# Kernel optimization log

Measured on AMD Instinct MI355X. Metric: run time of the kernel, lower is better.

Reference implementation:

```python
import jax, jax.numpy as jnp
import numpy as np

DIM = 1024
HEADS = 16
HEAD_DIM = DIM // HEADS
B, N = 2, 2048


def setup_inputs() -> dict:
    key = jax.random.key(0)
    ks = jax.random.split(key, 5)
    s = 1.0 / np.sqrt(DIM)
    return {
        "x": jax.random.normal(ks[0], (B, N, DIM), dtype=jnp.float32),
        "W_qkv": jax.random.uniform(ks[1], (DIM, 3 * DIM), jnp.float32, -s, s),
        "b_qkv": jax.random.uniform(ks[2], (3 * DIM,), jnp.float32, -s, s),
        "W_out": jax.random.uniform(ks[3], (DIM, DIM), jnp.float32, -s, s),
        "b_out": jax.random.uniform(ks[4], (DIM,), jnp.float32, -s, s),
    }


def reference(x, W_qkv, b_qkv, W_out, b_out):
    Bx, Nx, D = x.shape
    qkv = x @ W_qkv + b_qkv  # [B, N, 3D]
    qkv = qkv.reshape(Bx, Nx, 3, HEADS, HEAD_DIM)
    q, k, v = jnp.moveaxis(qkv, 2, 0)  # each [B, N, H, hd]
    q = jnp.swapaxes(q, 1, 2)  # [B, H, N, hd]
    k = jnp.swapaxes(k, 1, 2)
    v = jnp.swapaxes(v, 1, 2)
    scale = 1.0 / np.sqrt(HEAD_DIM)
    attn = jnp.einsum("bhqd,bhkd->bhqk", q, k) * scale  # [B, H, N, N]
    attn = jax.nn.softmax(attn, axis=-1)
    ctx = jnp.einsum("bhqk,bhkd->bhqd", attn, v)  # [B, H, N, hd]
    ctx = jnp.swapaxes(ctx, 1, 2).reshape(Bx, Nx, D)
    return ctx @ W_out + b_out
```

## Files before the change

### kernel.cpp

```cpp
#include <hip/hip_runtime.h>
#include <hip/hip_bf16.h>
#include <hip/hip_fp16.h>

#define DIMSZ 1024
#define HEADS 16
#define HD 64
#define BATCH 2
#define SEQ 2048
#define MROWS (BATCH*SEQ)

typedef _Float16 f16;
typedef _Float16 f16x8 __attribute__((ext_vector_type(8)));
typedef float f32x4 __attribute__((ext_vector_type(4)));

__device__ __forceinline__ void gload_lds16(const void* g, void* l) {
  __builtin_amdgcn_global_load_lds(
      (const __attribute__((address_space(1))) unsigned int*)g,
      (__attribute__((address_space(3))) unsigned int*)l, 16, 0, 0);
}

__global__ __launch_bounds__(256) void k_cvt_x(const float* __restrict__ in,
                                               f16* __restrict__ out) {
  int i = blockIdx.x * 256 + threadIdx.x;
  float4 v = ((const float4*)in)[i];
  union { f16 h[4]; uint2 u; } p;
  p.h[0] = (f16)v.x; p.h[1] = (f16)v.y; p.h[2] = (f16)v.z; p.h[3] = (f16)v.w;
  ((uint2*)out)[i] = p.u;
}

__global__ __launch_bounds__(256) void k_tcvt(const float* __restrict__ in,
                                              f16* __restrict__ out,
                                              int R, int C) {
  __shared__ f16 t[64][66];
  int c0 = blockIdx.x * 64, r0 = blockIdx.y * 64;
  int tid = threadIdx.x;
  int cc = tid & 63;
  #pragma unroll
  for (int p = 0; p < 16; p++) {
    int r = p * 4 + (tid >> 6);
    t[r][cc] = (f16)in[(size_t)(r0 + r) * C + c0 + cc];
  }
  __syncthreads();
  int rr = tid & 63;
  #pragma unroll
  for (int p = 0; p < 16; p++) {
    int c = p * 4 + (tid >> 6);
    out[(size_t)(c0 + c) * R + r0 + rr] = t[rr][c];
  }
}

#define GEMM_CORE(Aptr, Bptr)                                                  \
  __shared__ __align__(16) f16 As[128 * 64];                                   \
  __shared__ __align__(16) f16 Bs[128 * 64];                                   \
  const int K = 1024;                                                          \
  int tid = threadIdx.x, l = tid & 63, w = tid >> 6;                           \
  int bm = blockIdx.y, bn = blockIdx.x;                                        \
  int wr = (w >> 1) * 64, wc = (w & 1) * 64;                                   \
  const f16* Ag = (Aptr) + (size_t)bm * 128 * K;                               \
  const f16* Bg = (Bptr) + (size_t)bn * 128 * K;                               \
  f32x4 acc[4][4] = {};                                                        \
  for (int kt = 0; kt < K; kt += 64) {                                         \
    __syncthreads();                                                           \
    _Pragma("unroll")                                                          \
    for (int i = 0; i < 4; i++) {                                              \
      int base = i * 256 + w * 64;                                             \
      int chunk = base + l;                                                    \
      int row = chunk >> 3, c = chunk & 7, sc = c ^ (row & 7);                 \
      gload_lds16(Ag + (size_t)row * K + kt + sc * 8, &As[base * 8]);          \
    }                                                                          \
    _Pragma("unroll")                                                          \
    for (int i = 0; i < 4; i++) {                                              \
      int base = i * 256 + w * 64;                                             \
      int chunk = base + l;                                                    \
      int row = chunk >> 3, c = chunk & 7, sc = c ^ (row & 7);                 \
      gload_lds16(Bg + (size_t)row * K + kt + sc * 8, &Bs[base * 8]);          \
    }                                                                          \
    __syncthreads();                                                           \
    f16x8 af[4][2], bf[4][2];                                                  \
    _Pragma("unroll")                                                          \
    for (int m = 0; m < 4; m++)                                                \
      _Pragma("unroll")                                                        \
      for (int kk = 0; kk < 2; kk++) {                                         \
        int row = wr + m * 16 + (l & 15);                                      \
        int pc = (kk * 4 + (l >> 4)) ^ (row & 7);                              \
        af[m][kk] = *(const f16x8*)&As[row * 64 + pc * 8];                     \
      }                                                                        \
    _Pragma("unroll")                                                          \
    for (int n = 0; n < 4; n++)                                                \
      _Pragma("unroll")                                                        \
      for (int kk = 0; kk < 2; kk++) {                                         \
        int row = wc + n * 16 + (l & 15);                                      \
        int pc = (kk * 4 + (l >> 4)) ^ (row & 7);                              \
        bf[n][kk] = *(const f16x8*)&Bs[row * 64 + pc * 8];                     \
      }                                                                        \
    _Pragma("unroll")                                                          \
    for (int m = 0; m < 4; m++)                                                \
      _Pragma("unroll")                                                        \
      for (int n = 0; n < 4; n++)                                              \
        _Pragma("unroll")                                                      \
        for (int kk = 0; kk < 2; kk++)                                         \
          acc[m][n] = __builtin_amdgcn_mfma_f32_16x16x32_f16(af[m][kk],        \
                          bf[n][kk], acc[m][n], 0, 0, 0);                      \
  }

__global__ __launch_bounds__(256) void k_gemm_qkv(
    const f16* __restrict__ A, const f16* __restrict__ Bt,
    const float* __restrict__ bias,
    f16* __restrict__ qb, f16* __restrict__ kb, f16* __restrict__ vb) {
  GEMM_CORE(A, Bt)
  int gm0 = bm * 128 + wr;
  int gn0 = bn * 128 + wc;
  #pragma unroll
  for (int n = 0; n < 4; n++) {
    int col = gn0 + n * 16 + (l & 15);
    float bv = bias[col];
    int which = col >> 10, rest = col & 1023, h = rest >> 6, d = rest & 63;
    #pragma unroll
    for (int m = 0; m < 4; m++) {
      int rowb = gm0 + m * 16 + ((l >> 4) << 2);
      int b = rowb >> 11, nn = rowb & 2047;
      if (which == 2) {
        union { f16 h[4]; uint2 u; } pk;
        #pragma unroll
        for (int j = 0; j < 4; j++) pk.h[j] = (f16)(acc[m][n][j] + bv);
        *(uint2*)(vb + ((size_t)(b * HEADS + h) * 64 + d) * SEQ + nn) = pk.u;
      } else {
        f16* dst = (which ? kb : qb) + ((size_t)(b * HEADS + h) * SEQ + nn) * 64 + d;
        #pragma unroll
        for (int j = 0; j < 4; j++) dst[(size_t)j * 64] = (f16)(acc[m][n][j] + bv);
      }
    }
  }
}

__global__ __launch_bounds__(256) void k_gemm_out(
    const f16* __restrict__ A, const f16* __restrict__ Bt,
    const float* __restrict__ bias, float* __restrict__ out) {
  GEMM_CORE(A, Bt)
  int gm0 = bm * 128 + wr;
  int gn0 = bn * 128 + wc;
  #pragma unroll
  for (int n = 0; n < 4; n++) {
    int col = gn0 + n * 16 + (l & 15);
    float bv = bias[col];
    #pragma unroll
    for (int m = 0; m < 4; m++) {
      int rowb = gm0 + m * 16 + ((l >> 4) << 2);
      #pragma unroll
      for (int j = 0; j < 4; j++)
        out[(size_t)(rowb + j) * DIMSZ + col] = acc[m][n][j] + bv;
    }
  }
}

__global__ __launch_bounds__(512) void k_attn(
    const f16* __restrict__ qb, const f16* __restrict__ kb,
    const f16* __restrict__ vb, f16* __restrict__ ctx) {
  __shared__ __align__(16) f16 Ks[2][64 * 64];
  __shared__ __align__(16) f16 Vs[2][64 * 64];
  __shared__ __align__(16) f16 Pl[8][16 * 64];
  int tid = threadIdx.x, l = tid & 63, w = tid >> 6;
  int g = l >> 4, q = l & 15;
  int bid = blockIdx.x;
  int qtile = bid & 15, bh = bid >> 4;
  const f16* Qg = qb + ((size_t)bh * SEQ + qtile * 128 + w * 16) * 64;
  const f16* Kg = kb + (size_t)bh * SEQ * 64;
  const f16* Vg = vb + (size_t)bh * 64 * SEQ;

  f16x8 qf[2];
  #pragma unroll
  for (int kk = 0; kk < 2; kk++)
    qf[kk] = *(const f16x8*)(Qg + (size_t)q * 64 + kk * 32 + g * 8);

  f32x4 o[4] = {};
  float mrun = -INFINITY, lrun = 0.f;
  const float SC = 0.125f * 1.44269504f;

  int srow = tid >> 3, scc = tid & 7;
  int ssc = scc ^ (srow & 7);
  const f16* Ksrc = Kg + (size_t)srow * 64 + ssc * 8;
  const f16* Vsrc = Vg + (size_t)srow * SEQ + ssc * 8;

#define ATTN_STAGE(t, b) do {                                   \
    gload_lds16(Ksrc + (size_t)(t) * 4096, &Ks[b][w * 512]);    \
    gload_lds16(Vsrc + (size_t)(t) * 64,   &Vs[b][w * 512]);    \
  } while (0)

  ATTN_STAGE(0, 0);
  __syncthreads();

  for (int t = 0; t < 32; t++) {
    int cur = t & 1;
    if (t < 31) ATTN_STAGE(t + 1, cur ^ 1);

    f16x8 kf[4][2];
    #pragma unroll
    for (int n = 0; n < 4; n++)
      #pragma unroll
      for (int kk = 0; kk < 2; kk++) {
        int row = n * 16 + q;
        int pc = (kk * 4 + g) ^ (row & 7);
        kf[n][kk] = *(const f16x8*)&Ks[cur][row * 64 + pc * 8];
      }
    f32x4 s[4] = {};
    #pragma unroll
    for (int n = 0; n < 4; n++)
      #pragma unroll
      for (int kk = 0; kk < 2; kk++)
        s[n] = __builtin_amdgcn_mfma_f32_16x16x32_f16(kf[n][kk], qf[kk], s[n],
                                                      0, 0, 0);
    float tm = -INFINITY;
    #pragma unroll
    for (int n = 0; n < 4; n++)
      #pragma unroll
      for (int j = 0; j < 4; j++) tm = fmaxf(tm, s[n][j]);
    tm = fmaxf(tm, __shfl_xor(tm, 16));
    tm = fmaxf(tm, __shfl_xor(tm, 32));
    float mnew = fmaxf(mrun, tm);
    float a = mnew * SC;
    float corr = __builtin_amdgcn_exp2f(mrun * SC - a);
    float ts = 0.f;
    #pragma unroll
    for (int n = 0; n < 4; n++)
      #pragma unroll
      for (int j = 0; j < 4; j++) {
        float pv = __builtin_amdgcn_exp2f(s[n][j] * SC - a);
        s[n][j] = pv;
        ts += pv;
      }
    ts += __shfl_xor(ts, 16);
    ts += __shfl_xor(ts, 32);
    lrun = lrun * corr + ts;
    mrun = mnew;
    #pragma unroll
    for (int nd = 0; nd < 4; nd++) o[nd] *= corr;

    #pragma unroll
    for (int n = 0; n < 4; n++) {
      union { f16 h4[4]; uint2 u; } pk;
      #pragma unroll
      for (int j = 0; j < 4; j++) pk.h4[j] = (f16)s[n][j];
      int c = 2 * n + (g >> 1);
      *(uint2*)&Pl[w][q * 64 + ((c ^ (q & 7)) * 8) + (g & 1) * 4] = pk.u;
    }
    asm volatile("s_waitcnt lgkmcnt(0)" ::: "memory");
    __builtin_amdgcn_sched_barrier(0);

    f16x8 pf[2], vf[4][2];
    #pragma unroll
    for (int kk = 0; kk < 2; kk++) {
      int c = kk * 4 + g;
      pf[kk] = *(const f16x8*)&Pl[w][q * 64 + ((c ^ (q & 7)) * 8)];
    }
    #pragma unroll
    for (int nd = 0; nd < 4; nd++)
      #pragma unroll
      for (int kk = 0; kk < 2; kk++) {
        int row = nd * 16 + q;
        int pc = (kk * 4 + g) ^ (row & 7);
        vf[nd][kk] = *(const f16x8*)&Vs[cur][row * 64 + pc * 8];
      }
    #pragma unroll
    for (int nd = 0; nd < 4; nd++)
      #pragma unroll
      for (int kk = 0; kk < 2; kk++)
        o[nd] = __builtin_amdgcn_mfma_f32_16x16x32_f16(vf[nd][kk], pf[kk],
                                                       o[nd], 0, 0, 0);
    __syncthreads();
  }

  float inv = 1.0f / lrun;
  int b = bh >> 4, h = bh & 15;
  size_t rowoff = ((size_t)(b * SEQ + qtile * 128 + w * 16 + q)) * DIMSZ + h * 64;
  #pragma unroll
  for (int nd = 0; nd < 4; nd++) {
    union { f16 h4[4]; uint2 u; } pk;
    #pragma unroll
    for (int j = 0; j < 4; j++) pk.h4[j] = (f16)(o[nd][j] * inv);
    *(uint2*)(ctx + rowoff + nd * 16 + g * 4) = pk.u;
  }
#undef ATTN_STAGE
}

extern "C" void kernel_launch(void* const* d_in, const int* in_sizes, int n_in,
                              void* d_out, int out_size, void* d_ws, size_t ws_size,
                              hipStream_t stream) {
  const float* x    = (const float*)d_in[0];
  const float* Wqkv = (const float*)d_in[1];
  const float* bqkv = (const float*)d_in[2];
  const float* Wout = (const float*)d_in[3];
  const float* bout = (const float*)d_in[4];
  float* out = (float*)d_out;
  char* ws = (char*)d_ws;

  f16* xh    = (f16*)(ws);
  f16* ctx   = xh;
  f16* wqkvt = (f16*)(ws + 8388608);
  f16* woutt = (f16*)(ws + 14680064);
  f16* qbuf  = (f16*)(ws + 16777216);
  f16* kbuf  = (f16*)(ws + 25165824);
  f16* vbuf  = (f16*)(ws + 33554432);

  k_cvt_x<<<4096, 256, 0, stream>>>(x, xh);
  k_tcvt<<<dim3(48, 16), 256, 0, stream>>>(Wqkv, wqkvt, DIMSZ, 3 * DIMSZ);
  k_tcvt<<<dim3(16, 16), 256, 0, stream>>>(Wout, woutt, DIMSZ, DIMSZ);
  k_gemm_qkv<<<dim3(24, 32), 256, 0, stream>>>(xh, wqkvt, bqkv, qbuf, kbuf, vbuf);
  k_attn<<<512, 512, 0, stream>>>(qbuf, kbuf, vbuf, ctx);
  k_gemm_out<<<dim3(8, 32), 256, 0, stream>>>(ctx, woutt, bout, out);
}
```

Measured before the change: 206.1 us.

## Rewrite attention with 32x32 MFMA tiles and register-resident P via permlane swap

The attention kernel now uses 4 waves of 32 query rows each, with 32x32x16 MFMA instructions in place of 16x16x32. The P matrix stays in registers: it is packed with cvt_pkrtz and rearranged with v_permlane32_swap, which removes the LDS round-trip and its waitcnt. It also skips the output rescale when the running max does not change and raises wave priority around the MFMA blocks. Fewer threads per block means each thread issues more global-to-LDS loads and uses more registers, and the lower thread count per CU may reduce latency hiding.

```diff
diff --git a/kernel.cpp b/kernel.cpp
--- a/kernel.cpp
+++ b/kernel.cpp
@@ -12,6 +12,7 @@
 typedef _Float16 f16;
 typedef _Float16 f16x8 __attribute__((ext_vector_type(8)));
 typedef float f32x4 __attribute__((ext_vector_type(4)));
+typedef float f32x16 __attribute__((ext_vector_type(16)));
 
 __device__ __forceinline__ void gload_lds16(const void* g, void* l) {
   __builtin_amdgcn_global_load_lds(
@@ -153,37 +154,41 @@
   }
 }
 
-__global__ __launch_bounds__(512) void k_attn(
+__global__ __launch_bounds__(256) void k_attn(
     const f16* __restrict__ qb, const f16* __restrict__ kb,
     const f16* __restrict__ vb, f16* __restrict__ ctx) {
   __shared__ __align__(16) f16 Ks[2][64 * 64];
   __shared__ __align__(16) f16 Vs[2][64 * 64];
-  __shared__ __align__(16) f16 Pl[8][16 * 64];
   int tid = threadIdx.x, l = tid & 63, w = tid >> 6;
-  int g = l >> 4, q = l & 15;
-  int bid = blockIdx.x;
-  int qtile = bid & 15, bh = bid >> 4;
-  const f16* Qg = qb + ((size_t)bh * SEQ + qtile * 128 + w * 16) * 64;
+  int lq = l & 31, hh = l >> 5;
+  int qtile = blockIdx.x & 15, bh = blockIdx.x >> 4;
+
   const f16* Kg = kb + (size_t)bh * SEQ * 64;
   const f16* Vg = vb + (size_t)bh * 64 * SEQ;
 
-  f16x8 qf[2];
-  #pragma unroll
-  for (int kk = 0; kk < 2; kk++)
-    qf[kk] = *(const f16x8*)(Qg + (size_t)q * 64 + kk * 32 + g * 8);
-
-  f32x4 o[4] = {};
+  const f16* Qrow = qb + ((size_t)bh * SEQ + qtile * 128 + w * 32 + lq) * 64;
+  f16x8 qf[4];
+  #pragma unroll
+  for (int st = 0; st < 4; st++)
+    qf[st] = *(const f16x8*)(Qrow + st * 16 + hh * 8);
+
+  f32x16 o0 = {}, o1 = {};
   float mrun = -INFINITY, lrun = 0.f;
   const float SC = 0.125f * 1.44269504f;
 
-  int srow = tid >> 3, scc = tid & 7;
-  int ssc = scc ^ (srow & 7);
-  const f16* Ksrc = Kg + (size_t)srow * 64 + ssc * 8;
-  const f16* Vsrc = Vg + (size_t)srow * SEQ + ssc * 8;
-
-#define ATTN_STAGE(t, b) do {                                   \
-    gload_lds16(Ksrc + (size_t)(t) * 4096, &Ks[b][w * 512]);    \
-    gload_lds16(Vsrc + (size_t)(t) * 64,   &Vs[b][w * 512]);    \
+  int ch0 = tid, ch1 = tid + 256;
+  int r0 = ch0 >> 3, c0 = (ch0 & 7) ^ (r0 & 7);
+  int r1 = ch1 >> 3, c1 = (ch1 & 7) ^ (r1 & 7);
+  const f16* K0 = Kg + (size_t)r0 * 64 + c0 * 8;
+  const f16* K1 = Kg + (size_t)r1 * 64 + c1 * 8;
+  const f16* V0 = Vg + (size_t)r0 * SEQ + c0 * 8;
+  const f16* V1 = Vg + (size_t)r1 * SEQ + c1 * 8;
+
+#define ATTN_STAGE(t, b) do {                                     \
+    gload_lds16(K0 + (size_t)(t) * 4096, &Ks[b][w * 512]);        \
+    gload_lds16(K1 + (size_t)(t) * 4096, &Ks[b][2048 + w * 512]); \
+    gload_lds16(V0 + (size_t)(t) * 64,   &Vs[b][w * 512]);        \
+    gload_lds16(V1 + (size_t)(t) * 64,   &Vs[b][2048 + w * 512]); \
   } while (0)
 
   ATTN_STAGE(0, 0);
@@ -193,91 +198,88 @@
     int cur = t & 1;
     if (t < 31) ATTN_STAGE(t + 1, cur ^ 1);
 
-    f16x8 kf[4][2];
-    #pragma unroll
-    for (int n = 0; n < 4; n++)
+    f32x16 s0 = {}, s1 = {};
+    __builtin_amdgcn_s_setprio(1);
+    #pragma unroll
+    for (int st = 0; st < 4; st++) {
+      int ch = st * 2 + hh;
+      int sw = (ch ^ (lq & 7)) * 8;
+      f16x8 ka0 = *(const f16x8*)&Ks[cur][lq * 64 + sw];
+      f16x8 ka1 = *(const f16x8*)&Ks[cur][(32 + lq) * 64 + sw];
+      s0 = __builtin_amdgcn_mfma_f32_32x32x16_f16(ka0, qf[st], s0, 0, 0, 0);
+      s1 = __builtin_amdgcn_mfma_f32_32x32x16_f16(ka1, qf[st], s1, 0, 0, 0);
+    }
+    __builtin_amdgcn_s_setprio(0);
+
+    float tm = -INFINITY;
+    #pragma unroll
+    for (int i = 0; i < 16; i++) tm = fmaxf(tm, fmaxf(s0[i], s1[i]));
+    tm = fmaxf(tm, __shfl_xor(tm, 32));
+    if (!__all(tm <= mrun)) {
+      float mnew = fmaxf(mrun, tm);
+      float corr = __builtin_amdgcn_exp2f(mrun * SC - mnew * SC);
+      lrun *= corr;
       #pragma unroll
-      for (int kk = 0; kk < 2; kk++) {
-        int row = n * 16 + q;
-        int pc = (kk * 4 + g) ^ (row & 7);
-        kf[n][kk] = *(const f16x8*)&Ks[cur][row * 64 + pc * 8];
-      }
-    f32x4 s[4] = {};
-    #pragma unroll
-    for (int n = 0; n < 4; n++)
-      #pragma unroll
-      for (int kk = 0; kk < 2; kk++)
-        s[n] = __builtin_amdgcn_mfma_f32_16x16x32_f16(kf[n][kk], qf[kk], s[n],
-                                                      0, 0, 0);
-    float tm = -INFINITY;
-    #pragma unroll
-    for (int n = 0; n < 4; n++)
-      #pragma unroll
-      for (int j = 0; j < 4; j++) tm = fmaxf(tm, s[n][j]);
-    tm = fmaxf(tm, __shfl_xor(tm, 16));
-    tm = fmaxf(tm, __shfl_xor(tm, 32));
-    float mnew = fmaxf(mrun, tm);
-    float a = mnew * SC;
-    float corr = __builtin_amdgcn_exp2f(mrun * SC - a);
+      for (int i = 0; i < 16; i++) { o0[i] *= corr; o1[i] *= corr; }
+      mrun = mnew;
+    }
+    float a = mrun * SC;
     float ts = 0.f;
     #pragma unroll
-    for (int n = 0; n < 4; n++)
-      #pragma unroll
-      for (int j = 0; j < 4; j++) {
-        float pv = __builtin_amdgcn_exp2f(s[n][j] * SC - a);
-        s[n][j] = pv;
-        ts += pv;
-      }
-    ts += __shfl_xor(ts, 16);
+    for (int i = 0; i < 16; i++) {
+      s0[i] = __builtin_amdgcn_exp2f(s0[i] * SC - a);
+      s1[i] = __builtin_amdgcn_exp2f(s1[i] * SC - a);
+      ts += s0[i] + s1[i];
+    }
     ts += __shfl_xor(ts, 32);
-    lrun = lrun * corr + ts;
-    mrun = mnew;
-    #pragma unroll
-    for (int nd = 0; nd < 4; nd++) o[nd] *= corr;
-
-    #pragma unroll
-    for (int n = 0; n < 4; n++) {
-      union { f16 h4[4]; uint2 u; } pk;
-      #pragma unroll
-      for (int j = 0; j < 4; j++) pk.h4[j] = (f16)s[n][j];
-      int c = 2 * n + (g >> 1);
-      *(uint2*)&Pl[w][q * 64 + ((c ^ (q & 7)) * 8) + (g & 1) * 4] = pk.u;
-    }
-    asm volatile("s_waitcnt lgkmcnt(0)" ::: "memory");
-    __builtin_amdgcn_sched_barrier(0);
-
-    f16x8 pf[2], vf[4][2];
-    #pragma unroll
-    for (int kk = 0; kk < 2; kk++) {
-      int c = kk * 4 + g;
-      pf[kk] = *(const f16x8*)&Pl[w][q * 64 + ((c ^ (q & 7)) * 8)];
-    }
-    #pragma unroll
-    for (int nd = 0; nd < 4; nd++)
-      #pragma unroll
-      for (int kk = 0; kk < 2; kk++) {
-        int row = nd * 16 + q;
-        int pc = (kk * 4 + g) ^ (row & 7);
-        vf[nd][kk] = *(const f16x8*)&Vs[cur][row * 64 + pc * 8];
-      }
-    #pragma unroll
-    for (int nd = 0; nd < 4; nd++)
-      #pragma unroll
-      for (int kk = 0; kk < 2; kk++)
-        o[nd] = __builtin_amdgcn_mfma_f32_16x16x32_f16(vf[nd][kk], pf[kk],
-                                                       o[nd], 0, 0, 0);
+    lrun += ts;
+
+    f16x8 pb[4];
+    #pragma unroll
+    for (int ks = 0; ks < 4; ks++) {
+      const f32x16& sv = (ks < 2) ? s0 : s1;
+      const int rb = (ks & 1) * 8;
+      uint c01, c23, c45, c67;
+      asm("v_cvt_pkrtz_f16_f32 %0, %1, %2" : "=v"(c01) : "v"(sv[rb + 0]), "v"(sv[rb + 1]));
+      asm("v_cvt_pkrtz_f16_f32 %0, %1, %2" : "=v"(c23) : "v"(sv[rb + 2]), "v"(sv[rb + 3]));
+      asm("v_cvt_pkrtz_f16_f32 %0, %1, %2" : "=v"(c45) : "v"(sv[rb + 4]), "v"(sv[rb + 5]));
+      asm("v_cvt_pkrtz_f16_f32 %0, %1, %2" : "=v"(c67) : "v"(sv[rb + 6]), "v"(sv[rb + 7]));
+      asm("v_permlane32_swap_b32 %0, %1" : "+v"(c01), "+v"(c45));
+      asm("v_permlane32_swap_b32 %0, %1" : "+v"(c23), "+v"(c67));
+      union { uint u[4]; f16x8 v; } pu;
+      pu.u[0] = c01; pu.u[1] = c23; pu.u[2] = c45; pu.u[3] = c67;
+      pb[ks] = pu.v;
+    }
+
+    __builtin_amdgcn_s_setprio(1);
+    #pragma unroll
+    for (int ks = 0; ks < 4; ks++) {
+      int ch = ks * 2 + hh;
+      int sw = (ch ^ (lq & 7)) * 8;
+      f16x8 va0 = *(const f16x8*)&Vs[cur][lq * 64 + sw];
+      f16x8 va1 = *(const f16x8*)&Vs[cur][(32 + lq) * 64 + sw];
+      o0 = __builtin_amdgcn_mfma_f32_32x32x16_f16(va0, pb[ks], o0, 0, 0, 0);
+      o1 = __builtin_amdgcn_mfma_f32_32x32x16_f16(va1, pb[ks], o1, 0, 0, 0);
+    }
+    __builtin_amdgcn_s_setprio(0);
+
     __syncthreads();
   }
 
   float inv = 1.0f / lrun;
   int b = bh >> 4, h = bh & 15;
-  size_t rowoff = ((size_t)(b * SEQ + qtile * 128 + w * 16 + q)) * DIMSZ + h * 64;
-  #pragma unroll
-  for (int nd = 0; nd < 4; nd++) {
-    union { f16 h4[4]; uint2 u; } pk;
-    #pragma unroll
-    for (int j = 0; j < 4; j++) pk.h4[j] = (f16)(o[nd][j] * inv);
-    *(uint2*)(ctx + rowoff + nd * 16 + g * 4) = pk.u;
+  f16* crow = ctx + ((size_t)(b * SEQ + qtile * 128 + w * 32 + lq)) * DIMSZ
+              + h * 64 + 4 * hh;
+  #pragma unroll
+  for (int gsub = 0; gsub < 4; gsub++) {
+    union { f16 h4[4]; uint2 u; } p0, p1;
+    #pragma unroll
+    for (int j = 0; j < 4; j++) {
+      p0.h4[j] = (f16)(o0[gsub * 4 + j] * inv);
+      p1.h4[j] = (f16)(o1[gsub * 4 + j] * inv);
+    }
+    *(uint2*)(crow + gsub * 8) = p0.u;
+    *(uint2*)(crow + 32 + gsub * 8) = p1.u;
   }
 #undef ATTN_STAGE
 }
@@ -305,6 +307,6 @@
   k_tcvt<<<dim3(48, 16), 256, 0, stream>>>(Wqkv, wqkvt, DIMSZ, 3 * DIMSZ);
   k_tcvt<<<dim3(16, 16), 256, 0, stream>>>(Wout, woutt, DIMSZ, DIMSZ);
   k_gemm_qkv<<<dim3(24, 32), 256, 0, stream>>>(xh, wqkvt, bqkv, qbuf, kbuf, vbuf);
-  k_attn<<<512, 512, 0, stream>>>(qbuf, kbuf, vbuf, ctx);
+  k_attn<<<512, 256, 0, stream>>>(qbuf, kbuf, vbuf, ctx);
   k_gemm_out<<<dim3(8, 32), 256, 0, stream>>>(ctx, woutt, bout, out);
 }
```

After: 227.1 us. 10.2% more time.
